# Kernel optimization log

Measured on AMD Instinct MI355X. Metric: run time of the kernel, lower is better.

## Reference

```python
import jax, jax.numpy as jnp
import numpy as np

OBS = 64      # observation_dim = numel of one frame (1*8*8)
EXTRA = 20    # extra_hidden_dim
HID = OBS + EXTRA  # 84
T = 64        # sequence length
B = 16        # batch
L2 = 1e-3     # l2_regularization


def setup_inputs() -> dict:
    key = jax.random.key(0)
    k1, k2, k3 = jax.random.split(key, 3)
    # xavier_uniform-style init for A and C
    A = jax.random.uniform(k1, (HID, HID), minval=-1.0, maxval=1.0) * np.sqrt(6.0 / (HID + HID))
    C = jax.random.uniform(k2, (OBS, HID), minval=-1.0, maxval=1.0) * np.sqrt(6.0 / (OBS + HID))
    x = jax.random.normal(k3, (B, T, 1, 8, 8), dtype=jnp.float32)
    return {"x": x, "A": A.astype(jnp.float32), "C": C.astype(jnp.float32), "step": 0}


def build_M(A, C, seq_len):
    # T_reg = C with l2 added on its leading 'diagonal' entries C[k,k]
    d = jnp.arange(OBS)
    Treg = C.at[d, d].add(L2)
    # blocks[k] = Treg @ A^k, computed by a single scan (no Python loop over T^2)
    def step(carry, _):
        return carry @ A, carry
    _, blocks = jax.lax.scan(step, Treg, None, length=seq_len)  # [T, OBS, HID]
    i = jnp.arange(seq_len)
    diff = i[:, None] - i[None, :]                               # block (i,j) -> A-power i-j
    Mb = jnp.where((diff >= 0)[:, :, None, None],
                   blocks[jnp.clip(diff, 0, seq_len - 1)], 0.0)  # [T, T, OBS, HID]
    # block layout -> dense [T*OBS, T*HID]
    return Mb.transpose(0, 2, 1, 3).reshape(seq_len * OBS, seq_len * HID)


def reference(x, A, C, step):
    Bsz, seq_len = x.shape[0], x.shape[1]
    M = build_M(A, C, seq_len)                   # [T*OBS, T*HID]
    MMT = M @ M.T                                # [T*OBS, T*OBS]
    U = jnp.linalg.cholesky(MMT)                 # lower, as torch.potrf(upper=False)
    # The flow is an external invertible network; surrogate: identity flow, loss = 0
    zcat = x.reshape(Bsz, -1)                    # [B, T*OBS]
    Y = zcat
    z = jax.scipy.linalg.solve_triangular(U, Y.T, lower=True)          # U z = Y^T
    z = jax.scipy.linalg.solve_triangular(U, z, lower=True, trans='T')  # U^T z = z
    xe = (M.T @ z).T                             # [B, T*HID]
    eps = xe[:, HID:]                            # drop first hidden block
    prediction_loss = jnp.mean(eps * eps)        # + flow loss (0 for identity surrogate)
    return prediction_loss
```

## Files before the change

kernel.cpp:

```cpp
#include <hip/hip_runtime.h>

#define OBS 64
#define EXT 20
#define HID 84
#define TT  64
#define BB  16

#define OFF_T1INV 0
#define OFF_XT    4096
#define OFF_NA1   5376
#define OFF_ANT1  6656
#define OFF_ANA1  7936
#define OFF_N     9216
#define OFF_AN    10896
#define OFF_ICONV 12576
#define OFF_Q     13776
#define OFF_G     79312
#define OFF_JG    99792
#define OFF_ZG    125392
#define OFF_TS    150992
#define OFF_PART  171472

#define RDLANE(v, l) __uint_as_float(__builtin_amdgcn_readlane((int)__float_as_uint(v), (l)))

__device__ __forceinline__ void ld20(const float* p, float a[20]) {
    const float4* q = (const float4*)p;
    float4 v0 = q[0], v1 = q[1], v2 = q[2], v3 = q[3], v4 = q[4];
    a[0]=v0.x; a[1]=v0.y; a[2]=v0.z; a[3]=v0.w;
    a[4]=v1.x; a[5]=v1.y; a[6]=v1.z; a[7]=v1.w;
    a[8]=v2.x; a[9]=v2.y; a[10]=v2.z; a[11]=v2.w;
    a[12]=v3.x; a[13]=v3.y; a[14]=v3.z; a[15]=v3.w;
    a[16]=v4.x; a[17]=v4.y; a[18]=v4.z; a[19]=v4.w;
}

__device__ __forceinline__ float dot20(const float a[20], const float v[20]) {
    float s0 = 0.f, s1 = 0.f, s2 = 0.f, s3 = 0.f;
    #pragma unroll
    for (int m = 0; m < 20; m += 4) {
        s0 += a[m]     * v[m];
        s1 += a[m + 1] * v[m + 1];
        s2 += a[m + 2] * v[m + 2];
        s3 += a[m + 3] * v[m + 3];
    }
    return (s0 + s1) + (s2 + s3);
}

__device__ __forceinline__ void gj32_split(int lane, float w[32],
                                           float* __restrict__ sOut) {
    int r = lane & 31;
    bool mat = (lane < 32);
    bool used = false; int myk = 0;
    #pragma unroll
    for (int k = 0; k < 32; ++k) {
        float ak = __shfl(w[k], r);
        float v = (mat && !used) ? fabsf(ak) : -1.0f;
        int idx = r;
        #pragma unroll
        for (int off = 32; off; off >>= 1) {
            float v2 = __shfl_down(v, off);
            int   i2 = __shfl_down(idx, off);
            if (v2 > v) { v = v2; idx = i2; }
        }
        int p = __shfl(idx, 0);
        float piv = RDLANE(w[k], p);
        float rp  = 1.0f / piv;
        bool isp  = (r == p);
        float coeff = isp ? rp : -(ak * rp);
        if (mat && isp) { used = true; myk = k; }
        int psrc = p | (lane & 32);
        #pragma unroll
        for (int c = 0; c < 32; ++c) {
            float prc = __shfl(w[c], psrc);
            w[c] = isp ? (prc * rp) : fmaf(prc, coeff, w[c]);
        }
    }
    int myk2 = __shfl(myk, r);
    if (!mat) {
        #pragma unroll
        for (int c = 0; c < 32; ++c) sOut[myk2 * 32 + c] = w[c];
    }
}

__global__ __launch_bounds__(512) void k_prep(const float* __restrict__ A,
                                              const float* __restrict__ C,
                                              float* __restrict__ ws) {
    __shared__ float sPinv[1024], sW[1024], sV[1024], sSc[1024];
    __shared__ float sScinv[1024], sX1[1024], sX2[1024];
    __shared__ float Xs[64][20];
    __shared__ float Ns[84][20];
    __shared__ float ANs[84][20];
    __shared__ float sD[400], sDl[400], sF[400];
    int tid = threadIdx.x, wave = tid >> 6, lane = tid & 63;

    if (wave == 0) {
        int r = lane & 31;
        float w[32];
        #pragma unroll
        for (int c = 0; c < 32; ++c)
            w[c] = (lane < 32) ? (C[r * HID + c] + (c == r ? 1e-3f : 0.0f))
                               : ((c == r) ? 1.0f : 0.0f);
        gj32_split(lane, w, sPinv);
    }
    __syncthreads();

    for (int id = tid; id < 2048; id += 512) {
        int sel = id >> 10, rc = id & 1023, r = rc >> 5, c = rc & 31;
        float s = 0.f;
        if (sel == 0) {
            for (int m = 0; m < 32; ++m) s += C[(32 + r) * HID + m] * sPinv[m * 32 + c];
            sW[rc] = s;
        } else {
            for (int m = 0; m < 32; ++m) s += sPinv[r * 32 + m] * C[m * HID + 32 + c];
            sV[rc] = s;
        }
    }
    __syncthreads();

    for (int id = tid; id < 1024; id += 512) {
        int r = id >> 5, c = id & 31;
        float s = C[(32 + r) * HID + 32 + c] + (r == c ? 1e-3f : 0.f);
        for (int m = 0; m < 32; ++m) s -= sW[r * 32 + m] * C[m * HID + 32 + c];
        sSc[id] = s;
    }
    __syncthreads();

    if (wave == 0) {
        int r = lane & 31;
        float w[32];
        #pragma unroll
        for (int c = 0; c < 32; ++c)
            w[c] = (lane < 32) ? sSc[r * 32 + c] : ((c == r) ? 1.0f : 0.0f);
        gj32_split(lane, w, sScinv);
    }
    __syncthreads();

    for (int id = tid; id < 2048; id += 512) {
        int sel = id >> 10, rc = id & 1023, r = rc >> 5, c = rc & 31;
        float s = 0.f;
        if (sel == 0) {
            for (int m = 0; m < 32; ++m) s += sScinv[r * 32 + m] * sW[m * 32 + c];
            sX1[rc] = s;
        } else {
            for (int m = 0; m < 32; ++m) s += sV[r * 32 + m] * sScinv[m * 32 + c];
            sX2[rc] = s;
        }
    }
    __syncthreads();

    for (int id = tid; id < 1024; id += 512) {
        int r = id >> 5, c = id & 31;
        float x3 = 0.f;
        for (int m = 0; m < 32; ++m) x3 += sV[r * 32 + m] * sX1[m * 32 + c];
        ws[OFF_T1INV + r * 64 + c]              = sPinv[id] + x3;
        ws[OFF_T1INV + r * 64 + 32 + c]         = -sX2[id];
        ws[OFF_T1INV + (32 + r) * 64 + c]       = -sX1[id];
        ws[OFF_T1INV + (32 + r) * 64 + 32 + c]  = sScinv[id];
    }
    __syncthreads();

    for (int id = tid; id < 64 * 20; id += 512) {
        int r = id / 20, j = id % 20;
        float s = 0.f;
        const float* tr = ws + OFF_T1INV + r * 64;
        for (int c = 0; c < 64; ++c) s += tr[c] * C[c * HID + 64 + j];
        Xs[r][j] = s;
        ws[OFF_XT + j * 64 + r] = s;
    }
    __syncthreads();
    for (int id = tid; id < HID * 20; id += 512) {
        int p = id / 20, j = id % 20;
        float v = (p < 64) ? -Xs[p][j] : ((p - 64) == j ? 1.f : 0.f);
        Ns[p][j] = v;
        ws[OFF_N + id] = v;
    }
    __syncthreads();
    for (int id = tid; id < HID * 20; id += 512) {
        int p = id / 20, j = id % 20;
        float s = 0.f;
        for (int m = 0; m < HID; ++m) s += A[p * HID + m] * Ns[m][j];
        ANs[p][j] = s;
        ws[OFF_AN + id] = s;
    }
    __syncthreads();
    for (int id = tid; id < 400; id += 512) {
        int a = id / 20, b = id % 20;
        float sn = 0.f, sf = 0.f, sg = 0.f;
        for (int p = 0; p < HID; ++p) {
            sn += Ns[p][a] * Ns[p][b];
            sf += Ns[p][a] * ANs[p][b];
            sg += ANs[p][a] * ANs[p][b];
        }
        sF[id]  = sf;
        sD[id]  = sn + sg;
        sDl[id] = sn;
    }
    for (int id = tid; id < 20 * 64; id += 512) {
        int j = id / 64, c = id % 64;
        float s1 = 0.f, s2 = 0.f;
        for (int p = 0; p < HID; ++p) {
            float av = A[p * HID + c];
            s1 += Ns[p][j] * av;
            s2 += ANs[p][j] * av;
        }
        ws[OFF_NA1 + id]  = s1;
        ws[OFF_ANA1 + id] = s2;
        ws[OFF_ANT1 + id] = ANs[c][j];
    }
    __syncthreads();

    if (wave == 0) {
        float* Jg = ws + OFF_JG;
        float* Zg = ws + OFF_ZG;
        float Kprev[20];
        #pragma unroll
        for (int r = 0; r < 20; ++r) Kprev[r] = 0.f;
        int iconv = 62;
        for (int i = 0; i < 64; ++i) {
            bool last = (i == 63);
            float w[40];
            #pragma unroll
            for (int r = 0; r < 20; ++r) {
                float v, v2 = 0.f;
                if (lane < 20) {
                    float dv = last ? sDl[r * 20 + lane] : sD[r * 20 + lane];
                    v  = dv - Kprev[r];
                    v2 = sF[r * 20 + lane];
                } else if (lane < 40) {
                    v = sF[(lane - 20) * 20 + r];
                } else if (lane < 60) {
                    v = (r == lane - 40) ? 1.f : 0.f;
                } else {
                    v = 0.f;
                }
                w[r]      = v;
                w[20 + r] = v2;
            }
            #pragma unroll
            for (int k = 0; k < 20; ++k) {
                float rp = __builtin_amdgcn_rcpf(RDLANE(w[k], k));
                w[k] *= rp;
                #pragma unroll
                for (int r = 0; r < 40; ++r) {
                    if (r == k) continue;
                    float ck = RDLANE(w[r], k);
                    w[r] -= ck * w[k];
                }
            }
            if (lane >= 40 && lane < 60) {
                int c = lane - 40;
                #pragma unroll
                for (int r = 0; r < 20; ++r) {
                    Jg[i * 400 + r * 20 + c] = w[r];
                    if (!last) Zg[i * 400 + c * 20 + r] = -w[20 + r];
                }
            }
            if (last) break;
            float dmax = 0.f, kmax = 0.f;
            int gsel = (20 + lane) << 2;
            #pragma unroll
            for (int r = 0; r < 20; ++r) {
                float kn = -__uint_as_float(__builtin_amdgcn_ds_bpermute(
                    gsel, (int)__float_as_uint(w[20 + r])));
                dmax = fmaxf(dmax, fabsf(kn - Kprev[r]));
                kmax = fmaxf(kmax, fabsf(kn));
                Kprev[r] = kn;
            }
            if (i < 62 && __all((lane >= 20) || (dmax <= 1e-7f + 1e-4f * kmax))) {
                iconv = i;
                i = 62;
            }
        }
        if (lane == 0) ws[OFF_ICONV] = __int_as_float(iconv);
    }
}

__global__ __launch_bounds__(64) void k_qg(const float* __restrict__ x,
                                           float* __restrict__ ws) {
    int i = blockIdx.x, b = blockIdx.y, r = threadIdx.x;
    __shared__ float yv[3][64];
    __shared__ float qs[3][64];
    yv[1][r] = x[(b * TT + i) * 64 + r];
    yv[0][r] = (i > 0)  ? x[(b * TT + i - 1) * 64 + r] : 0.f;
    yv[2][r] = (i < 63) ? x[(b * TT + i + 1) * 64 + r] : 0.f;
    __syncthreads();
    const float* Ti = ws + OFF_T1INV + r * 64;
    float q0 = 0.f, q1 = 0.f, q2 = 0.f;
    for (int c = 0; c < 64; ++c) {
        float t = Ti[c];
        q0 += t * yv[0][c];
        q1 += t * yv[1][c];
        q2 += t * yv[2][c];
    }
    qs[0][r] = q0; qs[1][r] = q1; qs[2][r] = q2;
    ws[OFF_Q + (b * TT + i) * 64 + r] = q1;
    __syncthreads();
    if (r < 20) {
        const float* xt = ws + OFF_XT   + r * 64;
        const float* na = ws + OFF_NA1  + r * 64;
        const float* at = ws + OFF_ANT1 + r * 64;
        const float* aa = ws + OFF_ANA1 + r * 64;
        float s = 0.f;
        if (i < 63) {
            for (int c = 0; c < 64; ++c)
                s += xt[c] * qs[1][c] + na[c] * qs[0][c] + at[c] * qs[2][c] - aa[c] * qs[1][c];
        } else {
            for (int c = 0; c < 64; ++c)
                s += xt[c] * qs[1][c] + na[c] * qs[0][c];
        }
        ws[OFF_G + (i * 16 + b) * 20 + r] = s;
    }
}

__global__ __launch_bounds__(64, 1) void k_sweeps(float* __restrict__ ws) {
    __shared__ float rh[TT][2][20];
    __shared__ float th[2][20];
    int lane = threadIdx.x;
    int bh   = lane >> 5;
    int b    = (blockIdx.x << 1) + bh;
    int j    = lane & 31;
    int jj   = (j < 20) ? j : 0;
    bool actj = (j < 20);

    int icv = __float_as_int(ws[OFF_ICONV]);
    const float* G  = ws + OFF_G;
    const float* Jg = ws + OFF_JG;
    const float* Zg = ws + OFF_ZG;
    float* TS = ws + OFF_TS;

    float Mrow[20];
    #pragma unroll
    for (int m = 0; m < 20; ++m) Mrow[m] = Zg[icv * 400 + m * 20 + jj];
    float Jr[20], Zr[20], J63r[20];
    ld20(Jg + icv * 400 + jj * 20, Jr);
    ld20(Zg + icv * 400 + jj * 20, Zr);
    ld20(Jg + 63 * 400 + jj * 20, J63r);

    float rt = 0.f, gnext = 0.f;
    if (actj) {
        rt    = G[(0 * 16 + b) * 20 + j];
        rh[0][bh][j] = rt;
        gnext = G[(1 * 16 + b) * 20 + j];
    }
    for (int i = 1; i < TT; ++i) {
        float rv[20];
        ld20(&rh[i - 1][bh][0], rv);
        float s;
        if (i - 1 < icv) {
            float fr[20];
            #pragma unroll
            for (int m = 0; m < 20; ++m) fr[m] = Zg[(i - 1) * 400 + m * 20 + jj];
            s = gnext + dot20(fr, rv);
        } else {
            s = gnext + dot20(Mrow, rv);
        }
        rt = s;
        if (actj) {
            rh[i][bh][j] = rt;
            gnext = (i + 1 < TT) ? G[((i + 1) * 16 + b) * 20 + j] : 0.f;
        }
    }

    {
        float rv[20];
        ld20(&rh[63][bh][0], rv);
        float tn = dot20(J63r, rv);
        if (actj) {
            TS[(63 * 16 + b) * 20 + j] = tn;
            th[bh][j] = tn;
        }
        for (int i = 62; i >= 0; --i) {
            float rvi[20], tv[20];
            ld20(&rh[i][bh][0], rvi);
            ld20(&th[bh][0], tv);
            float t;
            if (i < icv) {
                float jr[20], zr[20];
                ld20(Jg + i * 400 + jj * 20, jr);
                ld20(Zg + i * 400 + jj * 20, zr);
                t = dot20(jr, rvi) + dot20(zr, tv);
            } else {
                t = dot20(Jr, rvi) + dot20(Zr, tv);
            }
            if (actj) {
                TS[(i * 16 + b) * 20 + j] = t;
                th[bh][j] = t;
            }
        }
    }
}

__global__ __launch_bounds__(128) void k_loss(const float* __restrict__ A,
                                              float* __restrict__ ws) {
    int i = blockIdx.x + 1, b = blockIdx.y, tid = threadIdx.x;
    __shared__ float ti[20], tm[20], qi[64], qm[64];
    __shared__ float red[128];
    if (tid < 20) {
        ti[tid] = ws[OFF_TS + (i * 16 + b) * 20 + tid];
        tm[tid] = ws[OFF_TS + ((i - 1) * 16 + b) * 20 + tid];
    }
    if (tid < 64) {
        qi[tid] = ws[OFF_Q + (b * TT + i) * 64 + tid];
        qm[tid] = ws[OFF_Q + (b * TT + i - 1) * 64 + tid];
    }
    __syncthreads();
    float e = 0.f;
    if (tid < HID) {
        int p = tid;
        float s = (p < 64) ? qi[p] : 0.f;
        const float* Np  = ws + OFF_N  + p * 20;
        const float* ANp = ws + OFF_AN + p * 20;
        for (int j = 0; j < 20; ++j) s += Np[j] * ti[j] - ANp[j] * tm[j];
        const float* Ar = A + p * HID;
        for (int c = 0; c < 64; ++c) s -= Ar[c] * qm[c];
        e = s * s;
    }
    red[tid] = e;
    __syncthreads();
    for (int off = 64; off; off >>= 1) {
        if (tid < off) red[tid] += red[tid + off];
        __syncthreads();
    }
    if (tid == 0) ws[OFF_PART + b * 63 + (i - 1)] = red[0];
}

__global__ __launch_bounds__(256) void k_reduce(const float* __restrict__ ws,
                                                float* __restrict__ out) {
    __shared__ float red[256];
    int tid = threadIdx.x;
    float s = 0.f;
    for (int id = tid; id < BB * 63; id += 256) s += ws[OFF_PART + id];
    red[tid] = s;
    __syncthreads();
    for (int off = 128; off; off >>= 1) {
        if (tid < off) red[tid] += red[tid + off];
        __syncthreads();
    }
    if (tid == 0) out[0] = red[0] / (float)(BB * (TT - 1) * HID);
}

extern "C" void kernel_launch(void* const* d_in, const int* in_sizes, int n_in,
                              void* d_out, int out_size, void* d_ws, size_t ws_size,
                              hipStream_t stream) {
    (void)in_sizes; (void)n_in; (void)out_size; (void)ws_size;
    const float* x = (const float*)d_in[0];
    const float* A = (const float*)d_in[1];
    const float* C = (const float*)d_in[2];
    float* ws  = (float*)d_ws;
    float* out = (float*)d_out;

    k_prep  <<<dim3(1),          dim3(512), 0, stream>>>(A, C, ws);
    k_qg    <<<dim3(TT, BB),     dim3(64),  0, stream>>>(x, ws);
    k_sweeps<<<dim3(8),          dim3(64),  0, stream>>>(ws);
    k_loss  <<<dim3(TT - 1, BB), dim3(128), 0, stream>>>(A, ws);
    k_reduce<<<dim3(1),          dim3(256), 0, stream>>>(ws, out);
}
```

Measured before the change: 187.1 us.

## Fuse qg, sweeps, loss and reduce into one persistent kernel with atomic barriers

Merges four dependent kernels into a single 1024-block kernel whose phases are separated by global atomic counters with spin-waits, and replaces the separate reduce kernel with a last-block-done final reduction. This is meant to cut launch overhead and inter-kernel gaps. It relies on all 1024 blocks being co-resident for the spin barriers, which risks deadlock if they are not. The counters are reset in k_prep, and the loss phase now uses wave shuffles instead of a shared-memory tree.

```diff
diff --git a/kernel.cpp b/kernel.cpp
--- a/kernel.cpp
+++ b/kernel.cpp
@@ -14,6 +14,7 @@
 #define OFF_N     9216
 #define OFF_AN    10896
 #define OFF_ICONV 12576
+#define OFF_CNT   12580
 #define OFF_Q     13776
 #define OFF_G     79312
 #define OFF_JG    99792
@@ -43,6 +44,12 @@
         s3 += a[m + 3] * v[m + 3];
     }
     return (s0 + s1) + (s2 + s3);
+}
+
+__device__ __forceinline__ void spin_until(int* p, int target) {
+    while (__hip_atomic_load(p, __ATOMIC_RELAXED, __HIP_MEMORY_SCOPE_AGENT) < target)
+        __builtin_amdgcn_s_sleep(16);
+    __threadfence();
 }
 
 __device__ __forceinline__ void gj32_split(int lane, float w[32],
@@ -91,6 +98,11 @@
     __shared__ float ANs[84][20];
     __shared__ float sD[400], sDl[400], sF[400];
     int tid = threadIdx.x, wave = tid >> 6, lane = tid & 63;
+
+    if (tid == 0) {
+        int* cnt = (int*)(ws + OFF_CNT);
+        cnt[0] = 0; cnt[1] = 0; cnt[2] = 0;
+    }
 
     if (wave == 0) {
         int r = lane & 31;
@@ -274,168 +286,177 @@
     }
 }
 
-__global__ __launch_bounds__(64) void k_qg(const float* __restrict__ x,
-                                           float* __restrict__ ws) {
-    int i = blockIdx.x, b = blockIdx.y, r = threadIdx.x;
-    __shared__ float yv[3][64];
-    __shared__ float qs[3][64];
-    yv[1][r] = x[(b * TT + i) * 64 + r];
-    yv[0][r] = (i > 0)  ? x[(b * TT + i - 1) * 64 + r] : 0.f;
-    yv[2][r] = (i < 63) ? x[(b * TT + i + 1) * 64 + r] : 0.f;
-    __syncthreads();
-    const float* Ti = ws + OFF_T1INV + r * 64;
-    float q0 = 0.f, q1 = 0.f, q2 = 0.f;
-    for (int c = 0; c < 64; ++c) {
-        float t = Ti[c];
-        q0 += t * yv[0][c];
-        q1 += t * yv[1][c];
-        q2 += t * yv[2][c];
-    }
-    qs[0][r] = q0; qs[1][r] = q1; qs[2][r] = q2;
-    ws[OFF_Q + (b * TT + i) * 64 + r] = q1;
-    __syncthreads();
-    if (r < 20) {
-        const float* xt = ws + OFF_XT   + r * 64;
-        const float* na = ws + OFF_NA1  + r * 64;
-        const float* at = ws + OFF_ANT1 + r * 64;
-        const float* aa = ws + OFF_ANA1 + r * 64;
+#define RH(i, bh, j) smem[((i) * 2 + (bh)) * 20 + (j)]
+#define TH(bh, j)    smem[2560 + (bh) * 20 + (j)]
+
+__global__ __launch_bounds__(64, 1) void k_tail(const float* __restrict__ x,
+                                                const float* __restrict__ A,
+                                                float* __restrict__ ws,
+                                                float* __restrict__ out) {
+    __shared__ float smem[2600];
+    int bid = blockIdx.x, lane = threadIdx.x;
+    int* cnt = (int*)(ws + OFF_CNT);
+
+    {
+        int i = bid & 63, b = bid >> 6;
+        float* yv0 = smem;       float* yv1 = smem + 64;  float* yv2 = smem + 128;
+        float* qs0 = smem + 192; float* qs1 = smem + 256; float* qs2 = smem + 320;
+        yv1[lane] = x[(b * TT + i) * 64 + lane];
+        yv0[lane] = (i > 0)  ? x[(b * TT + i - 1) * 64 + lane] : 0.f;
+        yv2[lane] = (i < 63) ? x[(b * TT + i + 1) * 64 + lane] : 0.f;
+        __syncthreads();
+        const float* Ti = ws + OFF_T1INV + lane * 64;
+        float q0 = 0.f, q1 = 0.f, q2 = 0.f;
+        for (int c = 0; c < 64; ++c) {
+            float t = Ti[c];
+            q0 += t * yv0[c];
+            q1 += t * yv1[c];
+            q2 += t * yv2[c];
+        }
+        qs0[lane] = q0; qs1[lane] = q1; qs2[lane] = q2;
+        ws[OFF_Q + (b * TT + i) * 64 + lane] = q1;
+        __syncthreads();
+        if (lane < 20) {
+            const float* xt = ws + OFF_XT   + lane * 64;
+            const float* na = ws + OFF_NA1  + lane * 64;
+            const float* at = ws + OFF_ANT1 + lane * 64;
+            const float* aa = ws + OFF_ANA1 + lane * 64;
+            float s = 0.f;
+            if (i < 63) {
+                for (int c = 0; c < 64; ++c)
+                    s += xt[c] * qs1[c] + na[c] * qs0[c] + at[c] * qs2[c] - aa[c] * qs1[c];
+            } else {
+                for (int c = 0; c < 64; ++c)
+                    s += xt[c] * qs1[c] + na[c] * qs0[c];
+            }
+            ws[OFF_G + (i * 16 + b) * 20 + lane] = s;
+        }
+        __syncthreads();
+        __threadfence();
+        if (lane == 0) atomicAdd(&cnt[0], 1);
+    }
+
+    if (bid < 8) {
+        spin_until(&cnt[0], 1024);
+        int bh = lane >> 5;
+        int b  = (bid << 1) + bh;
+        int j  = lane & 31;
+        int jj = (j < 20) ? j : 0;
+        bool actj = (j < 20);
+
+        int icv = __float_as_int(ws[OFF_ICONV]);
+        const float* G  = ws + OFF_G;
+        const float* Jg = ws + OFF_JG;
+        const float* Zg = ws + OFF_ZG;
+        float* TS = ws + OFF_TS;
+
+        float Mrow[20];
+        #pragma unroll
+        for (int m = 0; m < 20; ++m) Mrow[m] = Zg[icv * 400 + m * 20 + jj];
+        float Jr[20], Zr[20], J63r[20];
+        ld20(Jg + icv * 400 + jj * 20, Jr);
+        ld20(Zg + icv * 400 + jj * 20, Zr);
+        ld20(Jg + 63 * 400 + jj * 20, J63r);
+
+        float rt = 0.f, gnext = 0.f;
+        if (actj) {
+            rt = G[(0 * 16 + b) * 20 + j];
+            RH(0, bh, j) = rt;
+            gnext = G[(1 * 16 + b) * 20 + j];
+        }
+        __syncthreads();
+        for (int i = 1; i < TT; ++i) {
+            float rv[20];
+            ld20(&RH(i - 1, bh, 0), rv);
+            float s;
+            if (i - 1 < icv) {
+                float fr[20];
+                #pragma unroll
+                for (int m = 0; m < 20; ++m) fr[m] = Zg[(i - 1) * 400 + m * 20 + jj];
+                s = gnext + dot20(fr, rv);
+            } else {
+                s = gnext + dot20(Mrow, rv);
+            }
+            rt = s;
+            if (actj) {
+                RH(i, bh, j) = rt;
+                gnext = (i + 1 < TT) ? G[((i + 1) * 16 + b) * 20 + j] : 0.f;
+            }
+        }
+        {
+            float rv[20];
+            ld20(&RH(63, bh, 0), rv);
+            float tn = dot20(J63r, rv);
+            if (actj) {
+                TS[(63 * 16 + b) * 20 + j] = tn;
+                TH(bh, j) = tn;
+            }
+            for (int i = 62; i >= 0; --i) {
+                float rvi[20], tv[20];
+                ld20(&RH(i, bh, 0), rvi);
+                ld20(&TH(bh, 0), tv);
+                float t;
+                if (i < icv) {
+                    float jr[20], zr[20];
+                    ld20(Jg + i * 400 + jj * 20, jr);
+                    ld20(Zg + i * 400 + jj * 20, zr);
+                    t = dot20(jr, rvi) + dot20(zr, tv);
+                } else {
+                    t = dot20(Jr, rvi) + dot20(Zr, tv);
+                }
+                if (actj) {
+                    TS[(i * 16 + b) * 20 + j] = t;
+                    TH(bh, j) = t;
+                }
+            }
+        }
+        __syncthreads();
+        __threadfence();
+        if (lane == 0) atomicAdd(&cnt[1], 1);
+    }
+
+    spin_until(&cnt[1], 8);
+    if (bid < 1008) {
+        int li = 1 + (bid % 63), lb = bid / 63;
+        if (lane < 20) {
+            smem[lane]      = ws[OFF_TS + (li * 16 + lb) * 20 + lane];
+            smem[20 + lane] = ws[OFF_TS + ((li - 1) * 16 + lb) * 20 + lane];
+        }
+        smem[40 + lane] = ws[OFF_Q + (lb * TT + li - 1) * 64 + lane];
+        float qi_val    = ws[OFF_Q + (lb * TT + li) * 64 + lane];
+        __syncthreads();
+        float acc = 0.f;
+        #pragma unroll
+        for (int pass = 0; pass < 2; ++pass) {
+            int p = lane + pass * 64;
+            if (p < HID) {
+                float e = (p < 64) ? qi_val : 0.f;
+                const float* Np  = ws + OFF_N  + p * 20;
+                const float* ANp = ws + OFF_AN + p * 20;
+                for (int j = 0; j < 20; ++j)
+                    e += Np[j] * smem[j] - ANp[j] * smem[20 + j];
+                const float* Ar = A + p * HID;
+                for (int c = 0; c < 64; ++c) e -= Ar[c] * smem[40 + c];
+                acc += e * e;
+            }
+        }
+        #pragma unroll
+        for (int off = 32; off; off >>= 1) acc += __shfl_down(acc, off);
+        if (lane == 0) ws[OFF_PART + bid] = acc;
+    }
+    __threadfence();
+    int old = 0;
+    if (lane == 0) old = atomicAdd(&cnt[2], 1);
+    old = __shfl(old, 0);
+
+    if (old == 1023) {
+        __threadfence();
         float s = 0.f;
-        if (i < 63) {
-            for (int c = 0; c < 64; ++c)
-                s += xt[c] * qs[1][c] + na[c] * qs[0][c] + at[c] * qs[2][c] - aa[c] * qs[1][c];
-        } else {
-            for (int c = 0; c < 64; ++c)
-                s += xt[c] * qs[1][c] + na[c] * qs[0][c];
-        }
-        ws[OFF_G + (i * 16 + b) * 20 + r] = s;
-    }
-}
-
-__global__ __launch_bounds__(64, 1) void k_sweeps(float* __restrict__ ws) {
-    __shared__ float rh[TT][2][20];
-    __shared__ float th[2][20];
-    int lane = threadIdx.x;
-    int bh   = lane >> 5;
-    int b    = (blockIdx.x << 1) + bh;
-    int j    = lane & 31;
-    int jj   = (j < 20) ? j : 0;
-    bool actj = (j < 20);
-
-    int icv = __float_as_int(ws[OFF_ICONV]);
-    const float* G  = ws + OFF_G;
-    const float* Jg = ws + OFF_JG;
-    const float* Zg = ws + OFF_ZG;
-    float* TS = ws + OFF_TS;
-
-    float Mrow[20];
-    #pragma unroll
-    for (int m = 0; m < 20; ++m) Mrow[m] = Zg[icv * 400 + m * 20 + jj];
-    float Jr[20], Zr[20], J63r[20];
-    ld20(Jg + icv * 400 + jj * 20, Jr);
-    ld20(Zg + icv * 400 + jj * 20, Zr);
-    ld20(Jg + 63 * 400 + jj * 20, J63r);
-
-    float rt = 0.f, gnext = 0.f;
-    if (actj) {
-        rt    = G[(0 * 16 + b) * 20 + j];
-        rh[0][bh][j] = rt;
-        gnext = G[(1 * 16 + b) * 20 + j];
-    }
-    for (int i = 1; i < TT; ++i) {
-        float rv[20];
-        ld20(&rh[i - 1][bh][0], rv);
-        float s;
-        if (i - 1 < icv) {
-            float fr[20];
-            #pragma unroll
-            for (int m = 0; m < 20; ++m) fr[m] = Zg[(i - 1) * 400 + m * 20 + jj];
-            s = gnext + dot20(fr, rv);
-        } else {
-            s = gnext + dot20(Mrow, rv);
-        }
-        rt = s;
-        if (actj) {
-            rh[i][bh][j] = rt;
-            gnext = (i + 1 < TT) ? G[((i + 1) * 16 + b) * 20 + j] : 0.f;
-        }
-    }
-
-    {
-        float rv[20];
-        ld20(&rh[63][bh][0], rv);
-        float tn = dot20(J63r, rv);
-        if (actj) {
-            TS[(63 * 16 + b) * 20 + j] = tn;
-            th[bh][j] = tn;
-        }
-        for (int i = 62; i >= 0; --i) {
-            float rvi[20], tv[20];
-            ld20(&rh[i][bh][0], rvi);
-            ld20(&th[bh][0], tv);
-            float t;
-            if (i < icv) {
-                float jr[20], zr[20];
-                ld20(Jg + i * 400 + jj * 20, jr);
-                ld20(Zg + i * 400 + jj * 20, zr);
-                t = dot20(jr, rvi) + dot20(zr, tv);
-            } else {
-                t = dot20(Jr, rvi) + dot20(Zr, tv);
-            }
-            if (actj) {
-                TS[(i * 16 + b) * 20 + j] = t;
-                th[bh][j] = t;
-            }
-        }
-    }
-}
-
-__global__ __launch_bounds__(128) void k_loss(const float* __restrict__ A,
-                                              float* __restrict__ ws) {
-    int i = blockIdx.x + 1, b = blockIdx.y, tid = threadIdx.x;
-    __shared__ float ti[20], tm[20], qi[64], qm[64];
-    __shared__ float red[128];
-    if (tid < 20) {
-        ti[tid] = ws[OFF_TS + (i * 16 + b) * 20 + tid];
-        tm[tid] = ws[OFF_TS + ((i - 1) * 16 + b) * 20 + tid];
-    }
-    if (tid < 64) {
-        qi[tid] = ws[OFF_Q + (b * TT + i) * 64 + tid];
-        qm[tid] = ws[OFF_Q + (b * TT + i - 1) * 64 + tid];
-    }
-    __syncthreads();
-    float e = 0.f;
-    if (tid < HID) {
-        int p = tid;
-        float s = (p < 64) ? qi[p] : 0.f;
-        const float* Np  = ws + OFF_N  + p * 20;
-        const float* ANp = ws + OFF_AN + p * 20;
-        for (int j = 0; j < 20; ++j) s += Np[j] * ti[j] - ANp[j] * tm[j];
-        const float* Ar = A + p * HID;
-        for (int c = 0; c < 64; ++c) s -= Ar[c] * qm[c];
-        e = s * s;
-    }
-    red[tid] = e;
-    __syncthreads();
-    for (int off = 64; off; off >>= 1) {
-        if (tid < off) red[tid] += red[tid + off];
-        __syncthreads();
-    }
-    if (tid == 0) ws[OFF_PART + b * 63 + (i - 1)] = red[0];
-}
-
-__global__ __launch_bounds__(256) void k_reduce(const float* __restrict__ ws,
-                                                float* __restrict__ out) {
-    __shared__ float red[256];
-    int tid = threadIdx.x;
-    float s = 0.f;
-    for (int id = tid; id < BB * 63; id += 256) s += ws[OFF_PART + id];
-    red[tid] = s;
-    __syncthreads();
-    for (int off = 128; off; off >>= 1) {
-        if (tid < off) red[tid] += red[tid + off];
-        __syncthreads();
-    }
-    if (tid == 0) out[0] = red[0] / (float)(BB * (TT - 1) * HID);
+        for (int id = lane; id < 1008; id += 64) s += ws[OFF_PART + id];
+        #pragma unroll
+        for (int off = 32; off; off >>= 1) s += __shfl_down(s, off);
+        if (lane == 0) out[0] = s / (float)(BB * (TT - 1) * HID);
+    }
 }
 
 extern "C" void kernel_launch(void* const* d_in, const int* in_sizes, int n_in,
@@ -448,9 +469,6 @@
     float* ws  = (float*)d_ws;
     float* out = (float*)d_out;
 
-    k_prep  <<<dim3(1),          dim3(512), 0, stream>>>(A, C, ws);
-    k_qg    <<<dim3(TT, BB),     dim3(64),  0, stream>>>(x, ws);
-    k_sweeps<<<dim3(8),          dim3(64),  0, stream>>>(ws);
-    k_loss  <<<dim3(TT - 1, BB), dim3(128), 0, stream>>>(A, ws);
-    k_reduce<<<dim3(1),          dim3(256), 0, stream>>>(ws, out);
-}
+    k_prep<<<dim3(1),    dim3(512), 0, stream>>>(A, C, ws);
+    k_tail<<<dim3(1024), dim3(64),  0, stream>>>(x, A, ws, out);
+}
```

Measured after the change: 296.7 us. 58.6% more time.
